# Kernel tuning notes

Hardware: AMD Instinct MI355X
Metric: run time of the kernel (lower is better)

Reference implementation:

```python
import jax, jax.numpy as jnp
import numpy as np

D_MODEL = 2048
HEADDIM = 32
NHEADS = D_MODEL // HEADDIM  # 64
BLOCK = 256
EPS = 1e-4


def segsum(x):
    # x: (..., T) -> (..., T, T) stable segment sums, -inf above diagonal
    T = x.shape[-1]
    xe = jnp.broadcast_to(x[..., None], x.shape + (T,))  # (..., d, e)
    lower = jnp.tril(jnp.ones((T, T), dtype=bool), -1)
    xe = jnp.where(lower, xe, 0.0)
    s = jnp.cumsum(xe, axis=-2)
    incl = jnp.tril(jnp.ones((T, T), dtype=bool), 0)
    return jnp.where(incl, s, -jnp.inf)


def ssd_minimal_discrete(X, A, B, C, block_len):
    # X: (b, L, h, p); A: (b, L, h); B, C: (b, L, h, n). L % block_len == 0.
    b, Lm, h, p = X.shape
    c = Lm // block_len
    Xb = X.reshape(b, c, block_len, h, p)
    Bb = B.reshape(b, c, block_len, h, B.shape[-1])
    Cb = C.reshape(b, c, block_len, h, C.shape[-1])
    Ab = A.reshape(b, c, block_len, h).transpose(0, 3, 1, 2)  # (b, h, c, l)
    A_cumsum = jnp.cumsum(Ab, axis=-1)
    Lmat = jnp.exp(segsum(Ab))  # (b, h, c, l, s)
    # 1. intra-chunk (diagonal block) output
    Y_diag = jnp.einsum('bclhn,bcshn,bhcls,bcshp->bclhp', Cb, Bb, Lmat, Xb)
    # 2. per-chunk states
    decay_states = jnp.exp(A_cumsum[:, :, :, -1:] - A_cumsum)  # (b, h, c, l)
    states = jnp.einsum('bclhn,bhcl,bclhp->bchpn', Bb, decay_states, Xb)
    # 3. inter-chunk recurrence
    init = jnp.zeros_like(states[:, :1])
    states = jnp.concatenate([init, states], axis=1)  # (b, c+1, h, p, n)
    A_last = jnp.pad(A_cumsum[:, :, :, -1], ((0, 0), (0, 0), (1, 0)))  # (b, h, c+1)
    decay_chunk = jnp.exp(segsum(A_last))  # (b, h, c+1, c+1)
    new_states = jnp.einsum('bhzc,bchpn->bzhpn', decay_chunk, states)
    states_in, final_state = new_states[:, :-1], new_states[:, -1]
    # 4. state -> output within chunks
    state_decay_out = jnp.exp(A_cumsum)  # (b, h, c, l)
    Y_off = jnp.einsum('bclhn,bchpn,bhcl->bclhp', Cb, states_in, state_decay_out)
    Y = (Y_diag + Y_off).reshape(b, Lm, h, p)
    return Y, final_state


def setup_inputs() -> dict:
    key = jax.random.key(0)
    k1, k2 = jax.random.split(key)
    Bsz, Lfull, M = 2, 4096, 2048
    hidden_states = jax.random.normal(k1, (Bsz, M, D_MODEL), dtype=jnp.float32)
    # boundaries at even positions: exactly M boundaries per row, position 0 is a boundary
    boundary_mask = jnp.broadcast_to((jnp.arange(Lfull) % 2 == 0)[None, :], (Bsz, Lfull))
    boundary_prob = jax.random.uniform(k2, (Bsz, Lfull, 2), dtype=jnp.float32)
    mask = jnp.ones((Bsz, Lfull), dtype=bool)
    return {"hidden_states": hidden_states, "boundary_mask": boundary_mask,
            "boundary_prob": boundary_prob, "mask": mask}


def reference(hidden_states, boundary_mask, boundary_prob, mask):
    Bsz, Lfull = boundary_mask.shape
    M = hidden_states.shape[1]
    # select boundary-position probabilities, in order, first M
    p = jnp.clip(boundary_prob[..., -1].astype(jnp.float32), EPS, 1.0 - EPS)
    token_idx = jnp.arange(Lfull)[None, :] + (~boundary_mask).astype(jnp.int32) * Lfull
    order = jnp.argsort(token_idx, axis=1, stable=True)
    p_sel = jnp.take_along_axis(p, order[:, :M], axis=1)  # (B, M)
    dt = jnp.log(1.0 / (1.0 - p_sel))
    x = hidden_states.astype(jnp.float32) / dt[..., None]
    Xr = x.reshape(Bsz, M, NHEADS, HEADDIM)
    A_dt = -jnp.broadcast_to(dt[:, :, None], (Bsz, M, NHEADS))  # A = -1, A*dt
    B_ssd = jnp.broadcast_to(p_sel[:, :, None, None], (Bsz, M, NHEADS, 1))
    C_ssd = jnp.ones_like(B_ssd)
    out, _ = ssd_minimal_discrete(Xr, A_dt, B_ssd, C_ssd, BLOCK)
    out = out.reshape(Bsz, M, D_MODEL)
    # plug back: each uncompressed token reads the EMA value of its chunk
    plug = jnp.cumsum(boundary_mask.astype(jnp.int32), axis=1) - 1  # (B, L)
    out = jnp.take_along_axis(out, plug[:, :, None], axis=1)  # (B, L, d_model)
    return out
```

## Files before the change

kernel.cpp:

```cpp
#include <hip/hip_runtime.h>
#include <math.h>

#define BSZ    2
#define LFULL  4096
#define MLEN   2048
#define DMODEL 2048
#define CLIP_EPS 1e-4f
#define CCH    256
#define TCH    8

typedef float f4 __attribute__((ext_vector_type(4)));

__global__ __launch_bounds__(1024, 4) void mega_front(
    const float* __restrict__ hid, const int* __restrict__ bmask_raw,
    const float* __restrict__ bprob,
    int* __restrict__ Ls, int* __restrict__ Le,
    float* __restrict__ wA, float* __restrict__ eA,
    float* __restrict__ cde, float* __restrict__ G)
{
  const int tid = threadIdx.x;
  const int j   = tid & 3;
  const int c   = tid >> 2;
  const int bx  = blockIdx.x;
  const int b   = blockIdx.y;

  __shared__ int   s_sel[MLEN];
  __shared__ float s_P[CCH];
  __shared__ f4    s_S[CCH][4];
  __shared__ int   s_wtot[16];
  __shared__ int   s_mode, s_ntrue;

  const int d4 = bx * 4 + j;
  const int o  = b * MLEN + c * TCH;
  const f4* xp = (const f4*)hid + ((size_t)o * DMODEL >> 2) + d4;
  f4 xr[TCH];
  #pragma unroll
  for (int t = 0; t < TCH; ++t) xr[t] = xp[(size_t)t * (DMODEL / 4)];
  #pragma unroll
  for (int t = 0; t < TCH; ++t) asm volatile("" : "+v"(xr[t]));

  if (tid == 0) {
    unsigned w0 = ((const unsigned*)bmask_raw)[0];
    s_mode = (w0 <= 1u) ? 1 : 0;
  }
  __syncthreads();
  const int mode = s_mode;
  const unsigned char* bmask_u8 = (const unsigned char*)bmask_raw;

  const int PER  = LFULL / 1024;
  const int base = tid * PER;

  int cnt = 0;
  #pragma unroll
  for (int i = 0; i < PER; ++i) {
    const int L = base + i;
    const int v = mode ? (bmask_raw[b * LFULL + L] != 0)
                       : (bmask_u8[b * LFULL + L] != 0);
    cnt += v;
  }

  const int lane = tid & 63, wv = tid >> 6;
  int incl = cnt;
  #pragma unroll
  for (int off = 1; off < 64; off <<= 1) {
    const int v = __shfl_up(incl, off, 64);
    if (lane >= off) incl += v;
  }
  if (lane == 63) s_wtot[wv] = incl;
  __syncthreads();
  if (tid == 0) {
    int run = 0;
    #pragma unroll
    for (int w = 0; w < 16; ++w) { const int t = s_wtot[w]; s_wtot[w] = run; run += t; }
    s_ntrue = run;
  }
  __syncthreads();
  const int excl  = (incl - cnt) + s_wtot[wv];
  const int ntrue = s_ntrue;

  {
    int trun = excl;
    #pragma unroll
    for (int i = 0; i < PER; ++i) {
      const int L = base + i;
      const int v = mode ? (bmask_raw[b * LFULL + L] != 0)
                         : (bmask_u8[b * LFULL + L] != 0);
      if (v) {
        if (trun < MLEN) s_sel[trun] = L;
        ++trun;
      } else {
        const int f = L - trun;
        const int slot = ntrue + f;
        if (slot < MLEN) s_sel[slot] = L;
      }
    }
  }
  __syncthreads();

  float w[TCH], e[TCH], cd[TCH];
  {
    float run = 1.0f;
    #pragma unroll
    for (int t = 0; t < TCH; ++t) {
      const int L = s_sel[c * TCH + t];
      float p = bprob[((size_t)b * LFULL + L) * 2 + 1];
      p = fminf(fmaxf(p, CLIP_EPS), 1.0f - CLIP_EPS);
      const float dt = -log1pf(-p);
      w[t] = p / dt;
      e[t] = 1.0f - p;
      run *= e[t];
      cd[t] = run;
    }
  }

  f4 st = {0.f, 0.f, 0.f, 0.f};
  #pragma unroll
  for (int t = 0; t < TCH; ++t) {
    const f4 x = xr[t];
    st.x = fmaf(e[t], st.x, w[t] * x.x);
    st.y = fmaf(e[t], st.y, w[t] * x.y);
    st.z = fmaf(e[t], st.z, w[t] * x.z);
    st.w = fmaf(e[t], st.w, w[t] * x.w);
  }
  s_S[c][j] = st;
  if (j == 0) s_P[c] = cd[TCH - 1];
  __syncthreads();

  for (int dstep = 1; dstep < CCH; dstep <<= 1) {
    const float pc = s_P[c];
    float pd = 1.0f;
    f4 sd = {0.f, 0.f, 0.f, 0.f};
    if (c >= dstep) { pd = s_P[c - dstep]; sd = s_S[c - dstep][j]; }
    __syncthreads();
    if (c >= dstep) {
      f4 cur = s_S[c][j];
      cur.x = fmaf(pc, sd.x, cur.x);
      cur.y = fmaf(pc, sd.y, cur.y);
      cur.z = fmaf(pc, sd.z, cur.z);
      cur.w = fmaf(pc, sd.w, cur.w);
      s_S[c][j] = cur;
      if (j == 0) s_P[c] = pc * pd;
    }
    __syncthreads();
  }

  f4 H = {0.f, 0.f, 0.f, 0.f};
  if (c > 0) H = s_S[c - 1][j];

  ((f4*)G)[((size_t)(b * CCH + c) * DMODEL >> 2) + d4] = H;

  if (bx == 0 && j == 0) {
    const int nb = (ntrue < MLEN) ? ntrue : MLEN;
    #pragma unroll
    for (int t = 0; t < TCH; ++t) {
      const int g = c * TCH + t;
      wA[b * MLEN + g]  = w[t];
      eA[b * MLEN + g]  = e[t];
      cde[b * MLEN + g] = cd[t];
      int ls, le;
      if (nb == 0) {
        ls = (g == 0) ? 0 : LFULL;
        le = (g == 0) ? LFULL : LFULL;
      } else if (g < nb) {
        ls = (g == 0) ? 0 : s_sel[g];
        le = (g == nb - 1) ? LFULL : s_sel[g + 1];
      } else {
        ls = LFULL; le = LFULL;
      }
      Ls[b * MLEN + g] = ls;
      Le[b * MLEN + g] = le;
    }
  }
}

__global__ __launch_bounds__(256) void k3_out(
    const float* __restrict__ hid, const float* __restrict__ wA,
    const float* __restrict__ eA, const float* __restrict__ cde,
    const float* __restrict__ G,
    const int* __restrict__ Ls, const int* __restrict__ Le,
    float* __restrict__ out)
{
  const int tid = threadIdx.x;
  const int c = blockIdx.y;
  const int b = blockIdx.z;

  __shared__ float s_w[TCH], s_e[TCH], s_c[TCH];
  __shared__ int   s_ls[TCH], s_le[TCH];
  const int o = b * MLEN + c * TCH;
  if (tid < TCH)          { s_w[tid] = wA[o + tid];  s_ls[tid] = Ls[o + tid]; }
  else if (tid < 2 * TCH) { const int t = tid - TCH;     s_e[t] = eA[o + t]; s_le[t] = Le[o + t]; }
  else if (tid < 3 * TCH) { const int t = tid - 2 * TCH; s_c[t] = cde[o + t]; }
  __syncthreads();

  const int d4 = blockIdx.x * 256 + tid;

  const f4 H = ((const f4*)G)[((size_t)(b * CCH + c) * DMODEL >> 2) + d4];

  const f4* xp = (const f4*)hid + ((size_t)(b * MLEN + c * TCH) * DMODEL >> 2) + d4;
  f4*       op = (f4*)out + ((size_t)b * LFULL * DMODEL >> 2) + d4;

  f4 st = {0.f, 0.f, 0.f, 0.f};
  #pragma unroll
  for (int t = 0; t < TCH; ++t) {
    const f4 x = xp[(size_t)t * (DMODEL / 4)];
    const float w = s_w[t], e = s_e[t], cd = s_c[t];
    st.x = fmaf(e, st.x, w * x.x);
    st.y = fmaf(e, st.y, w * x.y);
    st.z = fmaf(e, st.z, w * x.z);
    st.w = fmaf(e, st.w, w * x.w);
    f4 y;
    y.x = fmaf(cd, H.x, st.x);
    y.y = fmaf(cd, H.y, st.y);
    y.z = fmaf(cd, H.z, st.z);
    y.w = fmaf(cd, H.w, st.w);
    const int ls = s_ls[t], le = s_le[t];
    for (int L = ls; L < le; ++L) {
      __builtin_nontemporal_store(y, op + (size_t)L * (DMODEL / 4));
    }
  }
}

extern "C" void kernel_launch(void* const* d_in, const int* in_sizes, int n_in,
                              void* d_out, int out_size, void* d_ws, size_t ws_size,
                              hipStream_t stream) {
  const float* hid   = (const float*)d_in[0];
  const int*   bmask = (const int*)d_in[1];
  const float* bprob = (const float*)d_in[2];
  float*       out   = (float*)d_out;

  char* ws = (char*)d_ws;
  const size_t SZI = (size_t)BSZ * MLEN * sizeof(int);
  const size_t SZF = (size_t)BSZ * MLEN * sizeof(float);
  int*   Ls  = (int*)(ws);
  int*   Le  = (int*)(ws + SZI);
  float* wA  = (float*)(ws + 2 * SZI);
  float* eA  = (float*)(ws + 2 * SZI + SZF);
  float* cde = (float*)(ws + 2 * SZI + 2 * SZF);
  float* G   = (float*)(ws + 2 * SZI + 3 * SZF + 4096);

  mega_front<<<dim3(DMODEL / 16, BSZ), dim3(1024), 0, stream>>>(
      hid, bmask, bprob, Ls, Le, wA, eA, cde, G);

  k3_out<<<dim3(2, CCH, BSZ), dim3(256), 0, stream>>>(
      hid, wA, eA, cde, G, Ls, Le, out);
}
```

Measured before the change: 121.7 us.

## Split chunk scan into two halves with carry fixup in output kernel

The front kernel now scans 128 chunks per block instead of 256, with 8 float4 lanes per chunk, and splits the sequence into two halves across blockIdx.y. The first half's final state and the second half's cumulative decay products are written out. The output kernel then adds the carried state to chunks in the second half. This shortens the serial shared-memory scan and changes the grid shape. In exchange, each front block repeats the mask scan and adds extra small global reads in the output kernel.

```diff
diff --git a/kernel.cpp b/kernel.cpp
--- a/kernel.cpp
+++ b/kernel.cpp
@@ -8,29 +8,33 @@
 #define CLIP_EPS 1e-4f
 #define CCH    256
 #define TCH    8
+#define HCH    128
 
 typedef float f4 __attribute__((ext_vector_type(4)));
 
-__global__ __launch_bounds__(1024, 4) void mega_front(
+__global__ __launch_bounds__(1024, 4) void front(
     const float* __restrict__ hid, const int* __restrict__ bmask_raw,
     const float* __restrict__ bprob,
     int* __restrict__ Ls, int* __restrict__ Le,
     float* __restrict__ wA, float* __restrict__ eA,
-    float* __restrict__ cde, float* __restrict__ G)
+    float* __restrict__ cde, float* __restrict__ Gp,
+    float* __restrict__ Ecar, float* __restrict__ cumP1)
 {
   const int tid = threadIdx.x;
-  const int j   = tid & 3;
-  const int c   = tid >> 2;
-  const int bx  = blockIdx.x;
-  const int b   = blockIdx.y;
+  const int j   = tid & 7;
+  const int cl  = tid >> 3;
+  const int s   = blockIdx.x;
+  const int h   = blockIdx.y;
+  const int b   = blockIdx.z;
+  const int c   = h * HCH + cl;
 
   __shared__ int   s_sel[MLEN];
-  __shared__ float s_P[CCH];
-  __shared__ f4    s_S[CCH][4];
+  __shared__ float s_P[HCH];
+  __shared__ f4    s_S[HCH][9];
   __shared__ int   s_wtot[16];
   __shared__ int   s_mode, s_ntrue;
 
-  const int d4 = bx * 4 + j;
+  const int d4 = s * 8 + j;
   const int o  = b * MLEN + c * TCH;
   const f4* xp = (const f4*)hid + ((size_t)o * DMODEL >> 2) + d4;
   f4 xr[TCH];
@@ -122,34 +126,39 @@
     st.z = fmaf(e[t], st.z, w[t] * x.z);
     st.w = fmaf(e[t], st.w, w[t] * x.w);
   }
-  s_S[c][j] = st;
-  if (j == 0) s_P[c] = cd[TCH - 1];
-  __syncthreads();
-
-  for (int dstep = 1; dstep < CCH; dstep <<= 1) {
-    const float pc = s_P[c];
+  s_S[cl][j] = st;
+  if (j == 0) s_P[cl] = cd[TCH - 1];
+  __syncthreads();
+
+  for (int dstep = 1; dstep < HCH; dstep <<= 1) {
+    const float pc = s_P[cl];
     float pd = 1.0f;
     f4 sd = {0.f, 0.f, 0.f, 0.f};
-    if (c >= dstep) { pd = s_P[c - dstep]; sd = s_S[c - dstep][j]; }
+    if (cl >= dstep) { pd = s_P[cl - dstep]; sd = s_S[cl - dstep][j]; }
     __syncthreads();
-    if (c >= dstep) {
-      f4 cur = s_S[c][j];
+    if (cl >= dstep) {
+      f4 cur = s_S[cl][j];
       cur.x = fmaf(pc, sd.x, cur.x);
       cur.y = fmaf(pc, sd.y, cur.y);
       cur.z = fmaf(pc, sd.z, cur.z);
       cur.w = fmaf(pc, sd.w, cur.w);
-      s_S[c][j] = cur;
-      if (j == 0) s_P[c] = pc * pd;
+      s_S[cl][j] = cur;
+      if (j == 0) s_P[cl] = pc * pd;
     }
     __syncthreads();
   }
 
-  f4 H = {0.f, 0.f, 0.f, 0.f};
-  if (c > 0) H = s_S[c - 1][j];
-
-  ((f4*)G)[((size_t)(b * CCH + c) * DMODEL >> 2) + d4] = H;
-
-  if (bx == 0 && j == 0) {
+  f4 Hx = {0.f, 0.f, 0.f, 0.f};
+  if (cl > 0) Hx = s_S[cl - 1][j];
+  ((f4*)Gp)[((size_t)(b * CCH + c) * DMODEL >> 2) + d4] = Hx;
+
+  if (h == 0 && cl == HCH - 1)
+    ((f4*)Ecar)[(b * (DMODEL / 4)) + d4] = s_S[HCH - 1][j];
+
+  if (h == 1 && s == 0 && j == 0)
+    cumP1[b * HCH + cl] = (cl == 0) ? 1.0f : s_P[cl - 1];
+
+  if (s == 0 && j == 0) {
     const int nb = (ntrue < MLEN) ? ntrue : MLEN;
     #pragma unroll
     for (int t = 0; t < TCH; ++t) {
@@ -176,7 +185,8 @@
 __global__ __launch_bounds__(256) void k3_out(
     const float* __restrict__ hid, const float* __restrict__ wA,
     const float* __restrict__ eA, const float* __restrict__ cde,
-    const float* __restrict__ G,
+    const float* __restrict__ Gp, const float* __restrict__ Ecar,
+    const float* __restrict__ cumP1,
     const int* __restrict__ Ls, const int* __restrict__ Le,
     float* __restrict__ out)
 {
@@ -194,7 +204,15 @@
 
   const int d4 = blockIdx.x * 256 + tid;
 
-  const f4 H = ((const f4*)G)[((size_t)(b * CCH + c) * DMODEL >> 2) + d4];
+  f4 H = ((const f4*)Gp)[((size_t)(b * CCH + c) * DMODEL >> 2) + d4];
+  if (c >= HCH) {
+    const float cp = cumP1[b * HCH + (c - HCH)];
+    const f4 Ev = ((const f4*)Ecar)[(b * (DMODEL / 4)) + d4];
+    H.x = fmaf(cp, Ev.x, H.x);
+    H.y = fmaf(cp, Ev.y, H.y);
+    H.z = fmaf(cp, Ev.z, H.z);
+    H.w = fmaf(cp, Ev.w, H.w);
+  }
 
   const f4* xp = (const f4*)hid + ((size_t)(b * MLEN + c * TCH) * DMODEL >> 2) + d4;
   f4*       op = (f4*)out + ((size_t)b * LFULL * DMODEL >> 2) + d4;
@@ -231,16 +249,18 @@
   char* ws = (char*)d_ws;
   const size_t SZI = (size_t)BSZ * MLEN * sizeof(int);
   const size_t SZF = (size_t)BSZ * MLEN * sizeof(float);
-  int*   Ls  = (int*)(ws);
-  int*   Le  = (int*)(ws + SZI);
-  float* wA  = (float*)(ws + 2 * SZI);
-  float* eA  = (float*)(ws + 2 * SZI + SZF);
-  float* cde = (float*)(ws + 2 * SZI + 2 * SZF);
-  float* G   = (float*)(ws + 2 * SZI + 3 * SZF + 4096);
-
-  mega_front<<<dim3(DMODEL / 16, BSZ), dim3(1024), 0, stream>>>(
-      hid, bmask, bprob, Ls, Le, wA, eA, cde, G);
+  int*   Ls    = (int*)(ws);
+  int*   Le    = (int*)(ws + SZI);
+  float* wA    = (float*)(ws + 2 * SZI);
+  float* eA    = (float*)(ws + 2 * SZI + SZF);
+  float* cde   = (float*)(ws + 2 * SZI + 2 * SZF);
+  float* cumP  = (float*)(ws + 2 * SZI + 3 * SZF);
+  float* Ecar  = (float*)(ws + 2 * SZI + 3 * SZF + 1024);
+  float* Gp    = (float*)(ws + 2 * SZI + 3 * SZF + 1024 + 16384 + 2048);
+
+  front<<<dim3(DMODEL / 32, 2, BSZ), dim3(1024), 0, stream>>>(
+      hid, bmask, bprob, Ls, Le, wA, eA, cde, Gp, Ecar, cumP);
 
   k3_out<<<dim3(2, CCH, BSZ), dim3(256), 0, stream>>>(
-      hid, wA, eA, cde, G, Ls, Le, out);
+      hid, wA, eA, cde, Gp, Ecar, cumP, Ls, Le, out);
 }
```

Measured after the change: 118.1 us. -2.9%, faster.
